# Optimization experiments

Measured on AMD Instinct MI355X. Metric: run time of the kernel, lower is better.

Reference implementation:

```python
import jax, jax.numpy as jnp
import numpy as np

K = 16
EPS = 1e-5

def _conv1x1(w, b, x):
    # w: [O, I], x: [B, I, N] -> [B, O, N]
    return jnp.einsum('oi,bin->bon', w, x) + b[None, :, None]

def _bn(g, be, m, v, x):
    # inference-mode batchnorm over channel dim of [B, C, N]
    inv = g / jnp.sqrt(v + EPS)
    return x * inv[None, :, None] + (be - m * inv)[None, :, None]

def setup_inputs() -> dict:
    key = jax.random.key(0)
    ks = jax.random.split(key, 16)
    B, C, N = 2, 128, 8192
    d = {}
    d['x'] = jax.random.normal(ks[0], (B, C, N), jnp.float32)
    d['xyz'] = jax.random.normal(ks[1], (B, N, 3), jnp.float32)
    def conv(k, o, i):
        k1, k2 = jax.random.split(k)
        s = 1.0 / np.sqrt(i)
        return (jax.random.uniform(k1, (o, i), jnp.float32, -s, s),
                jax.random.uniform(k2, (o,), jnp.float32, -s, s))
    def bn(k, c):
        return (jax.random.uniform(k, (c,), jnp.float32, 0.5, 1.5),
                jnp.zeros((c,), jnp.float32), jnp.zeros((c,), jnp.float32), jnp.ones((c,), jnp.float32))
    # boundary_net: 2C->C (bn,relu), C->C (bn,relu)
    d['bw1'], d['bb1'] = conv(ks[2], C, 2 * C)
    d['bn1g'], d['bn1b'], d['bn1m'], d['bn1v'] = bn(ks[3], C)
    d['bw2'], d['bb2'] = conv(ks[4], C, C)
    d['bn2g'], d['bn2b'], d['bn2m'], d['bn2v'] = bn(ks[5], C)
    # spatial_relation: 4->32 (bn,relu), 32->64
    d['sw1'], d['sb1'] = conv(ks[6], 32, 4)
    d['sbng'], d['sbnb'], d['sbnm'], d['sbnv'] = bn(ks[7], 32)
    d['sw2'], d['sb2'] = conv(ks[8], 64, 32)
    # attention: C+64 -> C//2 (bn,relu), C//2 -> C, sigmoid
    d['aw1'], d['ab1'] = conv(ks[9], C // 2, C + 64)
    d['abng'], d['abnb'], d['abnm'], d['abnv'] = bn(ks[10], C // 2)
    d['aw2'], d['ab2'] = conv(ks[11], C, C // 2)
    return d

def reference(x, xyz, bw1, bb1, bn1g, bn1b, bn1m, bn1v, bw2, bb2, bn2g, bn2b, bn2m, bn2v,
              sw1, sb1, sbng, sbnb, sbnm, sbnv, sw2, sb2,
              aw1, ab1, abng, abnb, abnm, abnv, aw2, ab2):
    B, C, N = x.shape
    # pairwise squared distances [B, N, N]
    xx = jnp.sum(xyz * xyz, axis=2)  # [B, N]
    dist = xx[:, :, None] + xx[:, None, :] - 2.0 * jnp.einsum('bnd,bmd->bnm', xyz, xyz)
    _, knn_idx = jax.lax.top_k(-dist, K)  # [B, N, K], K smallest distances
    # gather neighbor coords [B, N, K, 3]
    knn_xyz = jax.vmap(lambda p, i: p[i])(xyz, knn_idx)
    rel = knn_xyz - xyz[:, :, None, :]                  # [B, N, K, 3]
    rel_d = jnp.sqrt(jnp.sum(rel * rel, axis=-1))       # [B, N, K]
    mean_rel = jnp.mean(rel, axis=2).transpose(0, 2, 1)   # [B, 3, N]
    mean_d = jnp.mean(rel_d, axis=2)[:, None, :]           # [B, 1, N]
    spatial = jnp.concatenate([mean_rel, mean_d], axis=1)  # [B, 4, N]
    s = jax.nn.relu(_bn(sbng, sbnb, sbnm, sbnv, _conv1x1(sw1, sb1, spatial)))
    spatial_feat = _conv1x1(sw2, sb2, s)  # [B, 64, N]
    # gather neighbor features [B, C, N, K]
    knn_feat = jax.vmap(lambda xb, ib: xb[:, ib])(x, knn_idx)
    max_diff = jnp.max(knn_feat - x[:, :, :, None], axis=3)  # [B, C, N]
    bf = jnp.concatenate([x, max_diff], axis=1)  # [B, 2C, N]
    bf = jax.nn.relu(_bn(bn1g, bn1b, bn1m, bn1v, _conv1x1(bw1, bb1, bf)))
    boundary_feat = jax.nn.relu(_bn(bn2g, bn2b, bn2m, bn2v, _conv1x1(bw2, bb2, bf)))
    ai = jnp.concatenate([x, spatial_feat], axis=1)  # [B, C+64, N]
    a = jax.nn.relu(_bn(abng, abnb, abnm, abnv, _conv1x1(aw1, ab1, ai)))
    attn = jax.nn.sigmoid(_conv1x1(aw2, ab2, a))  # [B, C, N]
    return x + boundary_feat * attn
```

## Files before the change

kernel.cpp:

```cpp
#include <hip/hip_runtime.h>
#include <math.h>

#define NPTS  8192
#define NB    2
#define NTOT  (NPTS*NB)
#define GD    60
#define NCELL (GD*GD*GD)
#define TOTC  (NB*NCELL)
#define HCELL 0.2f
#define INVH  5.0f
#define ORGN  (-6.0f)
#define NN    8192
#define SCAN_CHUNK 1024
#define NBLK_SCAN  ((TOTC + SCAN_CHUNK - 1) / SCAN_CHUNK)
#define RSTART    2
#define RESC      4
#define SEL_CAP  1024

#define OFF_CNT     ((size_t)0)
#define OFF_OFFS    (OFF_CNT    + (size_t)TOTC*4)
#define OFF_CELLID  (OFF_OFFS   + (size_t)TOTC*4)
#define OFF_RANK    (OFF_CELLID + (size_t)NTOT*4)
#define OFF_SPOS    (OFF_RANK   + (size_t)NTOT*4)
#define OFF_KNN     (OFF_SPOS   + (size_t)NTOT*16)
#define OFF_SPATIAL (OFF_KNN    + (size_t)NTOT*16*4)
#define OFF_XT      (OFF_SPATIAL+ (size_t)NB*4*NPTS*4)
#define OFF_MD      (OFF_XT     + (size_t)NB*128*NPTS*4)
#define OFF_S1      (OFF_MD     + (size_t)NB*128*NPTS*4)
#define OFF_SF      (OFF_S1     + (size_t)NB*32*NPTS*4)
#define OFF_Y1      (OFF_SF     + (size_t)NB*64*NPTS*4)
#define OFF_Y2      (OFF_Y1     + (size_t)NB*128*NPTS*4)
#define OFF_A1      (OFF_Y2     + (size_t)NB*128*NPTS*4)
#define OFF_SC      (OFF_A1     + (size_t)NB*64*NPTS*4)
#define OFF_BSUM    (OFF_SC     + (size_t)1088*4)
#define OFF_BPRE    (OFF_BSUM   + (size_t)NBLK_SCAN*4)
#define OFF_RNG     (((OFF_BPRE + (size_t)NBLK_SCAN*4) + 15) & ~(size_t)15)

static __device__ __forceinline__ float sumsq3(float x, float y, float z) {
    return __fadd_rn(__fadd_rn(__fmul_rn(x, x), __fmul_rn(y, y)), __fmul_rn(z, z));
}
static __device__ __forceinline__ float pdist4(float qx, float qy, float qz, float qxx,
                                               float px, float py, float pz) {
    float pxx = sumsq3(px, py, pz);
    float dot = __fadd_rn(__fadd_rn(__fmul_rn(qx, px), __fmul_rn(qy, py)), __fmul_rn(qz, pz));
    return __fsub_rn(__fadd_rn(qxx, pxx), __fadd_rn(dot, dot));
}
static __device__ __forceinline__ unsigned fkey(float f) {
    unsigned b = __float_as_uint(f);
    return b ^ ((unsigned)(((int)b) >> 31) | 0x80000000u);
}
static __device__ __forceinline__ unsigned long long shflx64(unsigned long long v, int m) {
    unsigned lo = __shfl_xor((unsigned)v, m, 64);
    unsigned hi = __shfl_xor((unsigned)(v >> 32), m, 64);
    return ((unsigned long long)hi << 32) | lo;
}
static __device__ __forceinline__ int wave_scan_incl(int v, int lane) {
    #pragma unroll
    for (int d = 1; d < 64; d <<= 1) {
        int u = __shfl_up(v, d, 64);
        v += (lane >= d) ? u : 0;
    }
    return v;
}
static __device__ __forceinline__ unsigned long long tkmake(float m) {
    return ((unsigned long long)(fkey(__fsub_rn(__fmul_rn(m, m), 1e-4f)) + 1u)) << 27;
}

__global__ void cell_build(const float* __restrict__ xyz, int* __restrict__ cnt,
                           int* __restrict__ cellid, int* __restrict__ rank) {
    int t = blockIdx.x * 256 + threadIdx.x;
    if (t >= NTOT) return;
    const float* p = xyz + (size_t)t * 3;
    float x = p[0], y = p[1], z = p[2];
    int cx = min(GD - 1, max(0, (int)floorf((x - ORGN) * INVH)));
    int cy = min(GD - 1, max(0, (int)floorf((y - ORGN) * INVH)));
    int cz = min(GD - 1, max(0, (int)floorf((z - ORGN) * INVH)));
    int gcell = (t >> 13) * NCELL + (cz * GD + cy) * GD + cx;
    rank[t] = atomicAdd(&cnt[gcell], 1);
    cellid[t] = gcell;
}

__global__ __launch_bounds__(256) void scan_sums(const int* __restrict__ cnt, int* __restrict__ bsum) {
    __shared__ int red[256];
    int blk = blockIdx.x, t = threadIdx.x;
    int i0 = blk * SCAN_CHUNK + t * 4;
    int s = 0;
    if (i0 + 3 < TOTC) {
        int4 v = *(const int4*)(cnt + i0);
        s = v.x + v.y + v.z + v.w;
    } else {
        for (int j = 0; j < 4; ++j) if (i0 + j < TOTC) s += cnt[i0 + j];
    }
    red[t] = s;
    __syncthreads();
    for (int d = 128; d > 0; d >>= 1) {
        if (t < d) red[t] += red[t + d];
        __syncthreads();
    }
    if (t == 0) bsum[blk] = red[0];
}

__global__ __launch_bounds__(512) void scan_top(const int* __restrict__ bsum, int* __restrict__ bpre) {
    __shared__ int ps[512];
    int t = threadIdx.x;
    int v = (t < NBLK_SCAN) ? bsum[t] : 0;
    ps[t] = v;
    __syncthreads();
    for (int d = 1; d < 512; d <<= 1) {
        int u = 0;
        if (t >= d) u = ps[t - d];
        __syncthreads();
        ps[t] += u;
        __syncthreads();
    }
    if (t < NBLK_SCAN) bpre[t] = ps[t] - v;
}

__global__ __launch_bounds__(256) void scan_write(const int* __restrict__ cnt, const int* __restrict__ bpre,
                                                  int* __restrict__ offs, int2* __restrict__ rng) {
    __shared__ int ps[256];
    int blk = blockIdx.x, t = threadIdx.x;
    int i0 = blk * SCAN_CHUNK + t * 4;
    int a = 0, b = 0, c = 0, d = 0;
    if (i0 + 3 < TOTC) {
        int4 v = *(const int4*)(cnt + i0);
        a = v.x; b = v.y; c = v.z; d = v.w;
    } else {
        if (i0 + 0 < TOTC) a = cnt[i0 + 0];
        if (i0 + 1 < TOTC) b = cnt[i0 + 1];
        if (i0 + 2 < TOTC) c = cnt[i0 + 2];
        if (i0 + 3 < TOTC) d = cnt[i0 + 3];
    }
    int s = a + b + c + d;
    ps[t] = s;
    __syncthreads();
    for (int dd = 1; dd < 256; dd <<= 1) {
        int u = 0;
        if (t >= dd) u = ps[t - dd];
        __syncthreads();
        ps[t] += u;
        __syncthreads();
    }
    int base = bpre[blk] + ps[t] - s;
    if (i0 + 3 < TOTC) {
        offs[i0 + 0] = base;
        offs[i0 + 1] = base + a;
        offs[i0 + 2] = base + a + b;
        offs[i0 + 3] = base + a + b + c;
        *(int4*)(rng + i0)     = make_int4(base, base + a, base + a, base + a + b);
        *(int4*)(rng + i0 + 2) = make_int4(base + a + b, base + a + b + c,
                                           base + a + b + c, base + s);
    } else {
        if (i0 + 0 < TOTC) { offs[i0 + 0] = base;             rng[i0 + 0] = make_int2(base, base + a); }
        if (i0 + 1 < TOTC) { offs[i0 + 1] = base + a;         rng[i0 + 1] = make_int2(base + a, base + a + b); }
        if (i0 + 2 < TOTC) { offs[i0 + 2] = base + a + b;     rng[i0 + 2] = make_int2(base + a + b, base + a + b + c); }
        if (i0 + 3 < TOTC) { offs[i0 + 3] = base + a + b + c; rng[i0 + 3] = make_int2(base + a + b + c, base + s); }
    }
}

__global__ void scatter_k(const float* __restrict__ xyz, const int* __restrict__ cellid,
                          const int* __restrict__ rank, const int* __restrict__ offs,
                          float4* __restrict__ spos) {
    int t = blockIdx.x * 256 + threadIdx.x;
    if (t >= NTOT) return;
    const float* p = xyz + (size_t)t * 3;
    float x = p[0], y = p[1], z = p[2];
    int pos = offs[cellid[t]] + rank[t];
    spos[pos] = make_float4(x, y, z, __int_as_float(t & (NPTS - 1)));
}

__global__ __launch_bounds__(64) void knn_kernel(const float4* __restrict__ spos,
                                                 const int2* __restrict__ rng,
                                                 int* __restrict__ knn,
                                                 float* __restrict__ spatial) {
    __shared__ __align__(16) unsigned long long sel[SEL_CAP];
    __shared__ __align__(16) unsigned long long sel2[512];
    int lane = threadIdx.x;
    int bid  = blockIdx.x;
    int s = (bid & 7) * (NTOT / 8) + (bid >> 3);
    float4 q = spos[s];
    float qx = q.x, qy = q.y, qz = q.z;
    float qxx = sumsq3(qx, qy, qz);
    int b  = s >> 13;
    int nq = __float_as_int(q.w);
    int cx = min(GD - 1, max(0, (int)floorf((qx - ORGN) * INVH)));
    int cy = min(GD - 1, max(0, (int)floorf((qy - ORGN) * INVH)));
    int cz = min(GD - 1, max(0, (int)floorf((qz - ORGN) * INVH)));
    const int2* rg = rng + b * NCELL;

    float mlx = qx - (ORGN + (float)cx * HCELL);
    float mhx = (ORGN + (float)(cx + 1) * HCELL) - qx;
    float mly = qy - (ORGN + (float)cy * HCELL);
    float mhy = (ORGN + (float)(cy + 1) * HCELL) - qy;
    float mlz = qz - (ORGN + (float)cz * HCELL);
    float mhz = (ORGN + (float)(cz + 1) * HCELL) - qz;
    float margin0 = fminf(fminf(fminf(mlx, mhx), fminf(mly, mhy)), fminf(mlz, mhz));

    int tot = 0, ovf = 0;

    auto scan_ball = [&](int RB, float mfin, unsigned long long tkfin) {
        if (mfin <= 0.f) return;
        float mfin2 = mfin * mfin;
        int L = 2 * RB + 1, nrows = L * L;
        for (int r0 = 0; r0 < nrows; r0 += 64) {
            int nr = min(64, nrows - r0);
            int rr = r0 + lane;
            int num = 0, start = 0;
            if (rr < nrows) {
                int dzr = rr / L - RB, dyr = rr % L - RB;
                int zc = cz + dzr, yc = cy + dyr;
                if ((unsigned)zc < GD && (unsigned)yc < GD) {
                    float ylo = ORGN + (float)yc * HCELL;
                    float zlo = ORGN + (float)zc * HCELL;
                    float dyl = fmaxf(fmaxf(ylo - qy, qy - (ylo + HCELL)), 0.f);
                    float dzl = fmaxf(fmaxf(zlo - qz, qz - (zlo + HCELL)), 0.f);
                    float rem = mfin2 - dyl * dyl - dzl * dzl;
                    if (rem > -1e-4f) {
                        float xh = sqrtf(fmaxf(rem, 0.f)) + 1e-3f;
                        int xlo = max(0, (int)floorf((qx - xh - ORGN) * INVH));
                        int xhi = min(GD - 1, (int)floorf((qx + xh - ORGN) * INVH));
                        if (xlo <= xhi) {
                            int rowb = (zc * GD + yc) * GD;
                            start = rg[rowb + xlo].x;
                            num   = rg[rowb + xhi].y - start;
                        }
                    }
                }
            }
            int inc = wave_scan_incl(num, lane);
            int ctot = __shfl(inc, 63, 64);
            if (ctot == 0) continue;
            int excl = inc - num;
            auto eg = [&](int base, int& sv, float4& pv, bool& vld) {
                int t = base + lane;
                vld = t < ctot;
                int tc = vld ? t : (ctot - 1);
                int lo = 0, hi = nr - 1;
                #pragma unroll
                for (int st = 0; st < 6; ++st) {
                    int mid = (lo + hi + 1) >> 1;
                    int e = __shfl(excl, mid, 64);
                    bool g = (e <= tc);
                    lo = g ? mid : lo;
                    hi = g ? hi : (mid - 1);
                }
                sv = __shfl(start, lo, 64) + (tc - __shfl(excl, lo, 64));
                pv = spos[sv];
            };
            int s0; float4 p0; bool v0;
            eg(0, s0, p0, v0);
            for (int base = 0; base < ctot; base += 64) {
                int s1 = 0; float4 p1 = p0; bool v1 = false;
                if (base + 64 < ctot) eg(base + 64, s1, p1, v1);
                float d = pdist4(qx, qy, qz, qxx, p0.x, p0.y, p0.z);
                unsigned long long key = ((unsigned long long)fkey(d) << 27)
                                       | ((unsigned long long)(unsigned)__float_as_int(p0.w) << 14)
                                       | (unsigned)s0;
                bool pass = v0 && (key < tkfin);
                unsigned long long mk = __ballot(pass);
                int cnum = (int)__popcll(mk);
                if (tot + cnum > SEL_CAP) { ovf = 1; return; }
                if (pass) sel[tot + (int)__popcll(mk & ((1ULL << lane) - 1ULL))] = key;
                tot += cnum;
                s0 = s1; p0 = p1; v0 = v1;
            }
        }
    };

    auto count_below = [&](unsigned long long tk) {
        int c = 0;
        for (int t0 = 0; t0 < tot; t0 += 64) {
            int tt = t0 + lane;
            if (tt < tot) c += (sel[tt] < tk) ? 1 : 0;
        }
        for (int o = 32; o > 0; o >>= 1) c += __shfl_xor(c, o, 64);
        return c;
    };

    float mfin1 = margin0 + (float)RSTART * HCELL;
    unsigned long long tkf1 = (mfin1 > 0.f) ? tkmake(mfin1) : 0ULL;
    if (tkf1) scan_ball(RSTART, mfin1, tkf1);

    unsigned long long tkey_sel = ~0ULL;
    int csel = 0;
    bool have = false;
    if (!ovf && tot >= 16) {
        float mA = margin0 + 1.0f * HCELL;
        if (mA > 0.f) {
            unsigned long long tkA = tkmake(mA);
            int cA = count_below(tkA);
            if (cA >= 16) { tkey_sel = tkA; csel = cA; have = true; }
        }
        if (!have) { tkey_sel = ~0ULL; csel = tot; have = true; }
    }
    if (!have && !ovf) {
        tot = 0;
        float mfin4 = margin0 + (float)RESC * HCELL;
        unsigned long long tkf4 = (mfin4 > 0.f) ? tkmake(mfin4) : 0ULL;
        if (tkf4) scan_ball(RESC, mfin4, tkf4);
        if (!ovf && tot >= 16) {
            float mB = margin0 + (float)(RESC - 1) * HCELL;
            if (mB > 0.f) {
                unsigned long long tkB = tkmake(mB);
                int cB = count_below(tkB);
                if (cB >= 16) { tkey_sel = tkB; csel = cB; have = true; }
            }
            if (!have) { tkey_sel = ~0ULL; csel = tot; have = true; }
        }
    }

    if (!have) {
        const float LADR[16] = {0.35f, 0.4725f, 0.637875f, 0.86113125f,
                                1.1625272f, 1.5694117f, 2.1187058f, 2.8602529f,
                                3.8613414f, 5.2128109f, 7.0372947f, 9.5003478f,
                                12.825470f, 17.314384f, 23.374418f, 31.555464f};
        int sbase = b << 13;
        int cc[16];
        #pragma unroll
        for (int k = 0; k < 16; ++k) cc[k] = 0;
        for (int i0 = 0; i0 < NPTS; i0 += 64) {
            float4 p = spos[sbase + i0 + lane];
            float d = pdist4(qx, qy, qz, qxx, p.x, p.y, p.z);
            #pragma unroll
            for (int k = 0; k < 16; ++k) cc[k] += (d < LADR[k] * LADR[k]) ? 1 : 0;
        }
        #pragma unroll
        for (int k = 0; k < 16; ++k)
            for (int o = 32; o > 0; o >>= 1) cc[k] += __shfl_xor(cc[k], o, 64);
        float Tq = LADR[15] * LADR[15]; int cL = cc[15];
        #pragma unroll
        for (int k = 14; k >= 0; --k) if (cc[k] >= 16) { Tq = LADR[k] * LADR[k]; cL = cc[k]; }
        if (cL <= SEL_CAP) {
            tot = 0;
            for (int i0 = 0; i0 < NPTS; i0 += 64) {
                int idx = sbase + i0 + lane;
                float4 p = spos[idx];
                float d = pdist4(qx, qy, qz, qxx, p.x, p.y, p.z);
                bool pass = (d < Tq);
                unsigned long long key = ((unsigned long long)fkey(d) << 27)
                                       | ((unsigned long long)(unsigned)__float_as_int(p.w) << 14)
                                       | (unsigned)idx;
                unsigned long long mk = __ballot(pass);
                if (pass) sel[tot + (int)__popcll(mk & ((1ULL << lane) - 1ULL))] = key;
                tot += (int)__popcll(mk);
            }
            tkey_sel = ~0ULL;
            csel = tot;
        } else {
            unsigned long long* mybuf = sel + lane;
            unsigned long long minkey = ~0ULL, maxkey = 0;
            int nbuf = 0;
            for (int i = lane; i < NPTS; i += 64) {
                float4 p = spos[sbase + i];
                float d = pdist4(qx, qy, qz, qxx, p.x, p.y, p.z);
                unsigned long long key = ((unsigned long long)fkey(d) << 27)
                                       | ((unsigned long long)(unsigned)__float_as_int(p.w) << 14)
                                       | (unsigned)(sbase + i);
                if (nbuf < 16) {
                    mybuf[(size_t)nbuf * 64] = key;
                    ++nbuf;
                    minkey = (key < minkey) ? key : minkey;
                    maxkey = (key > maxkey) ? key : maxkey;
                } else if (key < maxkey) {
                    unsigned long long vmax = 0, v2 = 0;
                    int pmax = 0;
                    #pragma unroll
                    for (int j = 0; j < 16; ++j) {
                        unsigned long long v = mybuf[(size_t)j * 64];
                        if (v > vmax) { v2 = vmax; vmax = v; pmax = j; }
                        else if (v > v2) { v2 = v; }
                    }
                    mybuf[(size_t)pmax * 64] = key;
                    maxkey = (key > v2) ? key : v2;
                    minkey = (key < minkey) ? key : minkey;
                }
            }
            unsigned long long keep = ~0ULL;
            for (int k = 0; k < 16; ++k) {
                unsigned long long m = minkey;
                for (int o = 32; o > 0; o >>= 1) {
                    unsigned long long pv = shflx64(m, o);
                    m = (pv < m) ? pv : m;
                }
                unsigned long long bal = __ballot(minkey == m);
                int wl = __ffsll((long long)bal) - 1;
                if (lane == wl) {
                    int pos = 0;
                    for (int j = 0; j < nbuf; ++j) if (mybuf[(size_t)j * 64] == m) pos = j;
                    --nbuf;
                    mybuf[(size_t)pos * 64] = mybuf[(size_t)nbuf * 64];
                    unsigned long long nm = ~0ULL;
                    for (int j = 0; j < nbuf; ++j) {
                        unsigned long long v = mybuf[(size_t)j * 64];
                        nm = (v < nm) ? v : nm;
                    }
                    minkey = nm;
                }
                if (lane == k) keep = m;
            }
            float rx = 0.f, ry = 0.f, rz = 0.f, rd = 0.f;
            if (lane < 16) {
                int sp = (int)(keep & 0x3FFFu);
                int oi = (int)((keep >> 14) & 0x1FFFu);
                float4 p = spos[sp];
                rx = p.x - qx; ry = p.y - qy; rz = p.z - qz;
                rd = sqrtf(__fadd_rn(__fadd_rn(__fmul_rn(rx, rx), __fmul_rn(ry, ry)), __fmul_rn(rz, rz)));
                knn[(((size_t)b << 13) + nq) * 16 + lane] = oi;
            }
            for (int o = 8; o > 0; o >>= 1) {
                rx += __shfl_xor(rx, o, 64);
                ry += __shfl_xor(ry, o, 64);
                rz += __shfl_xor(rz, o, 64);
                rd += __shfl_xor(rd, o, 64);
            }
            if (lane == 0) {
                const float inv16 = 0.0625f;
                spatial[((size_t)b * 4 + 0) * NPTS + nq] = rx * inv16;
                spatial[((size_t)b * 4 + 1) * NPTS + nq] = ry * inv16;
                spatial[((size_t)b * 4 + 2) * NPTS + nq] = rz * inv16;
                spatial[((size_t)b * 4 + 3) * NPTS + nq] = rd * inv16;
            }
            return;
        }
    }

    const unsigned long long* src = sel;
    int m = tot;
    if (tkey_sel != ~0ULL && csel <= 512) {
        int w = 0;
        for (int t0 = 0; t0 < tot; t0 += 64) {
            int tt = t0 + lane;
            unsigned long long v = (tt < tot) ? sel[tt] : ~0ULL;
            bool pass = (tt < tot) && (v < tkey_sel);
            unsigned long long mk = __ballot(pass);
            if (pass) sel2[w + (int)__popcll(mk & ((1ULL << lane) - 1ULL))] = v;
            w += (int)__popcll(mk);
        }
        asm volatile("s_waitcnt lgkmcnt(0)" ::: "memory");
        __builtin_amdgcn_sched_barrier(0);
        src = sel2; m = w;
        tkey_sel = ~0ULL;
    }
    float rxs = 0.f, rys = 0.f, rzs = 0.f, rds = 0.f;
    for (int t0 = 0; t0 < m; t0 += 64) {
        int tt = t0 + lane;
        if (tt < m) {
            unsigned long long kt = src[tt];
            if (kt < tkey_sel) {
                int rr = 0;
                for (int j = 0; j < m; ++j) rr += (src[j] < kt) ? 1 : 0;
                if (rr < 16) {
                    int sp = (int)(kt & 0x3FFFu);
                    int oi = (int)((kt >> 14) & 0x1FFFu);
                    float4 p = spos[sp];
                    float dx = p.x - qx, dy = p.y - qy, dz = p.z - qz;
                    float dl = sqrtf(__fadd_rn(__fadd_rn(__fmul_rn(dx, dx), __fmul_rn(dy, dy)), __fmul_rn(dz, dz)));
                    knn[(((size_t)b << 13) + nq) * 16 + rr] = oi;
                    rxs += dx; rys += dy; rzs += dz; rds += dl;
                }
            }
        }
    }
    for (int o = 32; o > 0; o >>= 1) {
        rxs += __shfl_xor(rxs, o, 64);
        rys += __shfl_xor(rys, o, 64);
        rzs += __shfl_xor(rzs, o, 64);
        rds += __shfl_xor(rds, o, 64);
    }
    if (lane == 0) {
        const float inv16 = 0.0625f;
        spatial[((size_t)b * 4 + 0) * NPTS + nq] = rxs * inv16;
        spatial[((size_t)b * 4 + 1) * NPTS + nq] = rys * inv16;
        spatial[((size_t)b * 4 + 2) * NPTS + nq] = rzs * inv16;
        spatial[((size_t)b * 4 + 3) * NPTS + nq] = rds * inv16;
    }
}

__global__ void transpose_k(const float* __restrict__ x, float* __restrict__ xT) {
    __shared__ float tl[32][33];
    int b = blockIdx.z;
    int n0 = blockIdx.x * 32, c0 = blockIdx.y * 32;
    int tx = threadIdx.x, ty = threadIdx.y;
    const float* xb = x + (size_t)b * 128 * NN;
    float* xtb = xT + (size_t)b * NN * 128;
    for (int i = 0; i < 32; i += 8) tl[ty + i][tx] = xb[(size_t)(c0 + ty + i) * NN + n0 + tx];
    __syncthreads();
    for (int i = 0; i < 32; i += 8) xtb[(size_t)(n0 + ty + i) * 128 + c0 + tx] = tl[tx][ty + i];
}

__global__ __launch_bounds__(256) void md_k(const float* __restrict__ xT,
                                            const int* __restrict__ knn,
                                            float* __restrict__ md) {
    __shared__ int ki[8][16];
    __shared__ float smd[8][132];
    int b = blockIdx.y;
    int n0 = blockIdx.x * 8;
    int tid = threadIdx.x;
    if (tid < 128) ki[tid >> 4][tid & 15] = knn[(((size_t)b << 13) + n0 + (tid >> 4)) * 16 + (tid & 15)];
    __syncthreads();
    int nl = tid >> 5;
    int c4 = (tid & 31) * 4;
    const float* xb = xT + (size_t)b * NPTS * 128;
    float4 m = make_float4(-3.0e38f, -3.0e38f, -3.0e38f, -3.0e38f);
    #pragma unroll
    for (int k = 0; k < 16; ++k) {
        const float4 g = *(const float4*)(xb + (size_t)ki[nl][k] * 128 + c4);
        m.x = fmaxf(m.x, g.x); m.y = fmaxf(m.y, g.y); m.z = fmaxf(m.z, g.z); m.w = fmaxf(m.w, g.w);
    }
    const float4 own = *(const float4*)(xb + (size_t)(n0 + nl) * 128 + c4);
    m.x -= own.x; m.y -= own.y; m.z -= own.z; m.w -= own.w;
    *(float4*)(&smd[nl][c4]) = m;
    __syncthreads();
    for (int r = 0; r < 4; ++r) {
        int c = (tid >> 3) + 32 * r;
        int n2 = tid & 7;
        md[((size_t)b * 128 + c) * NN + n0 + n2] = smd[n2][c];
    }
}

__global__ void prep_k(const float* bb1, const float* g1, const float* be1, const float* m1, const float* v1,
                       const float* bb2, const float* g2, const float* be2, const float* m2, const float* v2,
                       const float* sb1, const float* gs,  const float* bes, const float* ms, const float* vs,
                       const float* sb2,
                       const float* ab1, const float* ga,  const float* bea, const float* ma, const float* va,
                       const float* ab2, float* sc) {
    int t = threadIdx.x;
    if (t < 128) {
        float i1 = g1[t] / sqrtf(v1[t] + 1e-5f);
        sc[t] = i1;        sc[128 + t] = bb1[t] * i1 + be1[t] - m1[t] * i1;
        float i2 = g2[t] / sqrtf(v2[t] + 1e-5f);
        sc[256 + t] = i2;  sc[384 + t] = bb2[t] * i2 + be2[t] - m2[t] * i2;
        sc[832 + t] = 1.0f; sc[960 + t] = ab2[t];
    }
    if (t < 32) {
        float is = gs[t] / sqrtf(vs[t] + 1e-5f);
        sc[512 + t] = is;  sc[544 + t] = sb1[t] * is + bes[t] - ms[t] * is;
    }
    if (t < 64) {
        sc[576 + t] = 1.0f; sc[640 + t] = sb2[t];
        float ia = ga[t] / sqrtf(va[t] + 1e-5f);
        sc[704 + t] = ia;  sc[768 + t] = ab1[t] * ia + bea[t] - ma[t] * ia;
    }
}

template <int O, int K, int TILE_N, int SPLIT, int ACT>
__global__ __launch_bounds__(256) void conv_bn(const float* __restrict__ srcA,
                                               const float* __restrict__ srcB,
                                               const float* __restrict__ W,
                                               const float* __restrict__ scale,
                                               const float* __restrict__ shift,
                                               float* __restrict__ out,
                                               const float* __restrict__ resx,
                                               const float* __restrict__ y2,
                                               float* __restrict__ dout) {
    constexpr int KC  = (K < 64) ? K : 64;
    constexpr int NT4 = TILE_N / 4;
    constexpr int O4  = O / 4;
    static_assert(NT4 * O4 == 256, "thread mapping");
    __shared__ float wT[KC][O + 4];
    __shared__ float inT[KC][TILE_N];
    int tid = threadIdx.x;
    int b = blockIdx.z;
    int n0 = blockIdx.x * TILE_N;
    int n_thr = tid % NT4;
    int o_thr = tid / NT4;
    float acc[4][4] = {{0.f, 0.f, 0.f, 0.f}, {0.f, 0.f, 0.f, 0.f}, {0.f, 0.f, 0.f, 0.f}, {0.f, 0.f, 0.f, 0.f}};

    for (int k0 = 0; k0 < K; k0 += KC) {
        for (int idx = tid; idx < KC * O; idx += 256) {
            int cc = idx % KC;
            int o  = idx / KC;
            wT[cc][o] = W[(size_t)o * K + k0 + cc];
        }
        for (int idx = tid; idx < KC * NT4; idx += 256) {
            int cc = idx / NT4;
            int nf = idx % NT4;
            int cg = k0 + cc;
            const float* src = (cg < SPLIT)
                ? (srcA + ((size_t)b * SPLIT + cg) * NN)
                : (srcB + ((size_t)b * (K - SPLIT) + (cg - SPLIT)) * NN);
            *(float4*)(&inT[cc][nf * 4]) = *(const float4*)(src + n0 + nf * 4);
        }
        __syncthreads();
        #pragma unroll 8
        for (int c = 0; c < KC; ++c) {
            float4 wv = *(const float4*)(&wT[c][o_thr * 4]);
            float4 iv = *(const float4*)(&inT[c][n_thr * 4]);
            acc[0][0] = fmaf(wv.x, iv.x, acc[0][0]); acc[0][1] = fmaf(wv.x, iv.y, acc[0][1]);
            acc[0][2] = fmaf(wv.x, iv.z, acc[0][2]); acc[0][3] = fmaf(wv.x, iv.w, acc[0][3]);
            acc[1][0] = fmaf(wv.y, iv.x, acc[1][0]); acc[1][1] = fmaf(wv.y, iv.y, acc[1][1]);
            acc[1][2] = fmaf(wv.y, iv.z, acc[1][2]); acc[1][3] = fmaf(wv.y, iv.w, acc[1][3]);
            acc[2][0] = fmaf(wv.z, iv.x, acc[2][0]); acc[2][1] = fmaf(wv.z, iv.y, acc[2][1]);
            acc[2][2] = fmaf(wv.z, iv.z, acc[2][2]); acc[2][3] = fmaf(wv.z, iv.w, acc[2][3]);
            acc[3][0] = fmaf(wv.w, iv.x, acc[3][0]); acc[3][1] = fmaf(wv.w, iv.y, acc[3][1]);
            acc[3][2] = fmaf(wv.w, iv.z, acc[3][2]); acc[3][3] = fmaf(wv.w, iv.w, acc[3][3]);
        }
        __syncthreads();
    }
    #pragma unroll
    for (int j = 0; j < 4; ++j) {
        int o = o_thr * 4 + j;
        float scv = scale[o], shv = shift[o];
        float4 v;
        v.x = fmaf(acc[j][0], scv, shv);
        v.y = fmaf(acc[j][1], scv, shv);
        v.z = fmaf(acc[j][2], scv, shv);
        v.w = fmaf(acc[j][3], scv, shv);
        size_t obase = ((size_t)b * O + o) * NN + n0 + n_thr * 4;
        if (ACT == 1) {
            v.x = fmaxf(v.x, 0.f); v.y = fmaxf(v.y, 0.f); v.z = fmaxf(v.z, 0.f); v.w = fmaxf(v.w, 0.f);
            *(float4*)(out + obase) = v;
        } else if (ACT == 2) {
            float4 xr = *(const float4*)(resx + obase);
            float4 yr = *(const float4*)(y2 + obase);
            v.x = xr.x + yr.x / (1.f + __expf(-v.x));
            v.y = xr.y + yr.y / (1.f + __expf(-v.y));
            v.z = xr.z + yr.z / (1.f + __expf(-v.z));
            v.w = xr.w + yr.w / (1.f + __expf(-v.w));
            *(float4*)(dout + obase) = v;
        } else {
            *(float4*)(out + obase) = v;
        }
    }
}

extern "C" void kernel_launch(void* const* d_in, const int* in_sizes, int n_in,
                              void* d_out, int out_size, void* d_ws, size_t ws_size,
                              hipStream_t stream) {
    (void)in_sizes; (void)n_in; (void)out_size; (void)ws_size;
    const float* x    = (const float*)d_in[0];
    const float* xyz  = (const float*)d_in[1];
    const float* bw1  = (const float*)d_in[2];
    const float* bb1  = (const float*)d_in[3];
    const float* bn1g = (const float*)d_in[4];
    const float* bn1b = (const float*)d_in[5];
    const float* bn1m = (const float*)d_in[6];
    const float* bn1v = (const float*)d_in[7];
    const float* bw2  = (const float*)d_in[8];
    const float* bb2  = (const float*)d_in[9];
    const float* bn2g = (const float*)d_in[10];
    const float* bn2b = (const float*)d_in[11];
    const float* bn2m = (const float*)d_in[12];
    const float* bn2v = (const float*)d_in[13];
    const float* sw1  = (const float*)d_in[14];
    const float* sb1  = (const float*)d_in[15];
    const float* sbng = (const float*)d_in[16];
    const float* sbnb = (const float*)d_in[17];
    const float* sbnm = (const float*)d_in[18];
    const float* sbnv = (const float*)d_in[19];
    const float* sw2  = (const float*)d_in[20];
    const float* sb2  = (const float*)d_in[21];
    const float* aw1  = (const float*)d_in[22];
    const float* ab1  = (const float*)d_in[23];
    const float* abng = (const float*)d_in[24];
    const float* abnb = (const float*)d_in[25];
    const float* abnm = (const float*)d_in[26];
    const float* abnv = (const float*)d_in[27];
    const float* aw2  = (const float*)d_in[28];
    const float* ab2  = (const float*)d_in[29];

    char* ws = (char*)d_ws;
    int*    cnt    = (int*)(ws + OFF_CNT);
    int*    offs   = (int*)(ws + OFF_OFFS);
    int*    cellid = (int*)(ws + OFF_CELLID);
    int*    rank   = (int*)(ws + OFF_RANK);
    float4* spos   = (float4*)(ws + OFF_SPOS);
    int*    knn    = (int*)(ws + OFF_KNN);
    float*  spat   = (float*)(ws + OFF_SPATIAL);
    float*  xT     = (float*)(ws + OFF_XT);
    float*  md     = (float*)(ws + OFF_MD);
    float*  s1b    = (float*)(ws + OFF_S1);
    float*  sfb    = (float*)(ws + OFF_SF);
    float*  y1b    = (float*)(ws + OFF_Y1);
    float*  y2b    = (float*)(ws + OFF_Y2);
    float*  a1b    = (float*)(ws + OFF_A1);
    float*  sc     = (float*)(ws + OFF_SC);
    int*    bsum   = (int*)(ws + OFF_BSUM);
    int*    bpre   = (int*)(ws + OFF_BPRE);
    int2*   rng    = (int2*)(ws + OFF_RNG);
    float*  dout   = (float*)d_out;

    hipMemsetAsync(cnt, 0, (size_t)TOTC * 4, stream);
    cell_build<<<dim3((NTOT + 255) / 256), 256, 0, stream>>>(xyz, cnt, cellid, rank);
    scan_sums<<<dim3(NBLK_SCAN), 256, 0, stream>>>(cnt, bsum);
    scan_top<<<dim3(1), 512, 0, stream>>>(bsum, bpre);
    scan_write<<<dim3(NBLK_SCAN), 256, 0, stream>>>(cnt, bpre, offs, rng);
    scatter_k<<<dim3((NTOT + 255) / 256), 256, 0, stream>>>(xyz, cellid, rank, offs, spos);
    knn_kernel<<<dim3(NTOT), 64, 0, stream>>>(spos, rng, knn, spat);
    transpose_k<<<dim3(NPTS / 32, 128 / 32, NB), dim3(32, 8), 0, stream>>>(x, xT);
    md_k<<<dim3(NPTS / 8, NB), 256, 0, stream>>>(xT, knn, md);
    prep_k<<<1, 128, 0, stream>>>(bb1, bn1g, bn1b, bn1m, bn1v,
                                  bb2, bn2g, bn2b, bn2m, bn2v,
                                  sb1, sbng, sbnb, sbnm, sbnv,
                                  sb2,
                                  ab1, abng, abnb, abnm, abnv,
                                  ab2, sc);
    conv_bn<32, 4, 128, 4, 1><<<dim3(NPTS / 128, 1, NB), 256, 0, stream>>>(
        spat, spat, sw1, sc + 512, sc + 544, s1b, nullptr, nullptr, nullptr);
    conv_bn<64, 32, 64, 32, 0><<<dim3(NPTS / 64, 1, NB), 256, 0, stream>>>(
        s1b, s1b, sw2, sc + 576, sc + 640, sfb, nullptr, nullptr, nullptr);
    conv_bn<128, 256, 32, 128, 1><<<dim3(NPTS / 32, 1, NB), 256, 0, stream>>>(
        x, md, bw1, sc + 0, sc + 128, y1b, nullptr, nullptr, nullptr);
    conv_bn<128, 128, 32, 128, 1><<<dim3(NPTS / 32, 1, NB), 256, 0, stream>>>(
        y1b, y1b, bw2, sc + 256, sc + 384, y2b, nullptr, nullptr, nullptr);
    conv_bn<64, 192, 64, 128, 1><<<dim3(NPTS / 64, 1, NB), 256, 0, stream>>>(
        x, sfb, aw1, sc + 704, sc + 768, a1b, nullptr, nullptr, nullptr);
    conv_bn<128, 64, 32, 64, 2><<<dim3(NPTS / 32, 1, NB), 256, 0, stream>>>(
        a1b, a1b, aw2, sc + 832, sc + 960, dout, x, y2b, dout);
}
```

Before: 326.0 us.

## Fuse back-to-back 1x1 conv pairs keeping intermediates in shared memory

Replaces the four separate conv_bn launches for the boundary and attention MLPs with two fused kernels. Each fused kernel computes the first conv+BN+ReLU into a shared-memory tile, then applies the second conv directly from that tile. This removes the global round-trip of the y1 and a1 intermediates and two kernel launches. The cost is larger shared-memory footprints (about 66KB for boundary), which may lower occupancy, plus reloading weights for every point tile.

```diff
diff --git a/kernel.cpp b/kernel.cpp
--- a/kernel.cpp
+++ b/kernel.cpp
@@ -549,10 +549,7 @@
                                                const float* __restrict__ W,
                                                const float* __restrict__ scale,
                                                const float* __restrict__ shift,
-                                               float* __restrict__ out,
-                                               const float* __restrict__ resx,
-                                               const float* __restrict__ y2,
-                                               float* __restrict__ dout) {
+                                               float* __restrict__ out) {
     constexpr int KC  = (K < 64) ? K : 64;
     constexpr int NT4 = TILE_N / 4;
     constexpr int O4  = O / 4;
@@ -609,18 +606,190 @@
         size_t obase = ((size_t)b * O + o) * NN + n0 + n_thr * 4;
         if (ACT == 1) {
             v.x = fmaxf(v.x, 0.f); v.y = fmaxf(v.y, 0.f); v.z = fmaxf(v.z, 0.f); v.w = fmaxf(v.w, 0.f);
-            *(float4*)(out + obase) = v;
-        } else if (ACT == 2) {
-            float4 xr = *(const float4*)(resx + obase);
-            float4 yr = *(const float4*)(y2 + obase);
+        }
+        *(float4*)(out + obase) = v;
+    }
+}
+
+#define FMA16(ACCV, WV, IV) \
+    ACCV[0][0] = fmaf(WV.x, IV.x, ACCV[0][0]); ACCV[0][1] = fmaf(WV.x, IV.y, ACCV[0][1]); \
+    ACCV[0][2] = fmaf(WV.x, IV.z, ACCV[0][2]); ACCV[0][3] = fmaf(WV.x, IV.w, ACCV[0][3]); \
+    ACCV[1][0] = fmaf(WV.y, IV.x, ACCV[1][0]); ACCV[1][1] = fmaf(WV.y, IV.y, ACCV[1][1]); \
+    ACCV[1][2] = fmaf(WV.y, IV.z, ACCV[1][2]); ACCV[1][3] = fmaf(WV.y, IV.w, ACCV[1][3]); \
+    ACCV[2][0] = fmaf(WV.z, IV.x, ACCV[2][0]); ACCV[2][1] = fmaf(WV.z, IV.y, ACCV[2][1]); \
+    ACCV[2][2] = fmaf(WV.z, IV.z, ACCV[2][2]); ACCV[2][3] = fmaf(WV.z, IV.w, ACCV[2][3]); \
+    ACCV[3][0] = fmaf(WV.w, IV.x, ACCV[3][0]); ACCV[3][1] = fmaf(WV.w, IV.y, ACCV[3][1]); \
+    ACCV[3][2] = fmaf(WV.w, IV.z, ACCV[3][2]); ACCV[3][3] = fmaf(WV.w, IV.w, ACCV[3][3])
+
+__global__ __launch_bounds__(256) void fused_boundary(const float* __restrict__ x,
+                                                      const float* __restrict__ md,
+                                                      const float* __restrict__ W1,
+                                                      const float* __restrict__ W2,
+                                                      const float* __restrict__ sc,
+                                                      float* __restrict__ y2b) {
+    __shared__ float wT[64][132];
+    __shared__ float inT[64][32];
+    __shared__ float y1t[128][32];
+    int tid = threadIdx.x;
+    int b = blockIdx.z;
+    int n0 = blockIdx.x * 32;
+    int n_thr = tid % 8;
+    int o_thr = tid / 8;
+    float acc[4][4] = {{0.f,0.f,0.f,0.f},{0.f,0.f,0.f,0.f},{0.f,0.f,0.f,0.f},{0.f,0.f,0.f,0.f}};
+
+    for (int k0 = 0; k0 < 256; k0 += 64) {
+        for (int idx = tid; idx < 64 * 128; idx += 256) {
+            int cc = idx % 64;
+            int o  = idx / 64;
+            wT[cc][o] = W1[(size_t)o * 256 + k0 + cc];
+        }
+        for (int idx = tid; idx < 64 * 8; idx += 256) {
+            int cc = idx / 8;
+            int nf = idx % 8;
+            int cg = k0 + cc;
+            const float* src = (cg < 128)
+                ? (x  + ((size_t)b * 128 + cg) * NN)
+                : (md + ((size_t)b * 128 + (cg - 128)) * NN);
+            *(float4*)(&inT[cc][nf * 4]) = *(const float4*)(src + n0 + nf * 4);
+        }
+        __syncthreads();
+        #pragma unroll 8
+        for (int c = 0; c < 64; ++c) {
+            float4 wv = *(const float4*)(&wT[c][o_thr * 4]);
+            float4 iv = *(const float4*)(&inT[c][n_thr * 4]);
+            FMA16(acc, wv, iv);
+        }
+        __syncthreads();
+    }
+    #pragma unroll
+    for (int j = 0; j < 4; ++j) {
+        int o = o_thr * 4 + j;
+        float scv = sc[o], shv = sc[128 + o];
+        float4 v;
+        v.x = fmaxf(fmaf(acc[j][0], scv, shv), 0.f);
+        v.y = fmaxf(fmaf(acc[j][1], scv, shv), 0.f);
+        v.z = fmaxf(fmaf(acc[j][2], scv, shv), 0.f);
+        v.w = fmaxf(fmaf(acc[j][3], scv, shv), 0.f);
+        *(float4*)(&y1t[o][n_thr * 4]) = v;
+    }
+    __syncthreads();
+
+    float a2[4][4] = {{0.f,0.f,0.f,0.f},{0.f,0.f,0.f,0.f},{0.f,0.f,0.f,0.f},{0.f,0.f,0.f,0.f}};
+    for (int k0 = 0; k0 < 128; k0 += 64) {
+        for (int idx = tid; idx < 64 * 128; idx += 256) {
+            int cc = idx % 64;
+            int o  = idx / 64;
+            wT[cc][o] = W2[(size_t)o * 128 + k0 + cc];
+        }
+        __syncthreads();
+        #pragma unroll 8
+        for (int c = 0; c < 64; ++c) {
+            float4 wv = *(const float4*)(&wT[c][o_thr * 4]);
+            float4 iv = *(const float4*)(&y1t[k0 + c][n_thr * 4]);
+            FMA16(a2, wv, iv);
+        }
+        __syncthreads();
+    }
+    #pragma unroll
+    for (int j = 0; j < 4; ++j) {
+        int o = o_thr * 4 + j;
+        float scv = sc[256 + o], shv = sc[384 + o];
+        float4 v;
+        v.x = fmaxf(fmaf(a2[j][0], scv, shv), 0.f);
+        v.y = fmaxf(fmaf(a2[j][1], scv, shv), 0.f);
+        v.z = fmaxf(fmaf(a2[j][2], scv, shv), 0.f);
+        v.w = fmaxf(fmaf(a2[j][3], scv, shv), 0.f);
+        *(float4*)(y2b + ((size_t)b * 128 + o) * NN + n0 + n_thr * 4) = v;
+    }
+}
+
+__global__ __launch_bounds__(256) void fused_attn(const float* __restrict__ x,
+                                                  const float* __restrict__ sfb,
+                                                  const float* __restrict__ W1,
+                                                  const float* __restrict__ W2,
+                                                  const float* __restrict__ sc,
+                                                  const float* __restrict__ y2b,
+                                                  float* __restrict__ dout) {
+    __shared__ float wT[64][68];
+    __shared__ float inT[64][64];
+    __shared__ float a1t[64][64];
+    int tid = threadIdx.x;
+    int b = blockIdx.z;
+    int n0 = blockIdx.x * 64;
+    int n_thr = tid % 16;
+    int o_thr = tid / 16;
+    float acc[4][4] = {{0.f,0.f,0.f,0.f},{0.f,0.f,0.f,0.f},{0.f,0.f,0.f,0.f},{0.f,0.f,0.f,0.f}};
+
+    for (int k0 = 0; k0 < 192; k0 += 64) {
+        for (int idx = tid; idx < 64 * 64; idx += 256) {
+            int cc = idx % 64;
+            int o  = idx / 64;
+            wT[cc][o] = W1[(size_t)o * 192 + k0 + cc];
+        }
+        for (int idx = tid; idx < 64 * 16; idx += 256) {
+            int cc = idx / 16;
+            int nf = idx % 16;
+            int cg = k0 + cc;
+            const float* src = (cg < 128)
+                ? (x   + ((size_t)b * 128 + cg) * NN)
+                : (sfb + ((size_t)b * 64 + (cg - 128)) * NN);
+            *(float4*)(&inT[cc][nf * 4]) = *(const float4*)(src + n0 + nf * 4);
+        }
+        __syncthreads();
+        #pragma unroll 8
+        for (int c = 0; c < 64; ++c) {
+            float4 wv = *(const float4*)(&wT[c][o_thr * 4]);
+            float4 iv = *(const float4*)(&inT[c][n_thr * 4]);
+            FMA16(acc, wv, iv);
+        }
+        __syncthreads();
+    }
+    #pragma unroll
+    for (int j = 0; j < 4; ++j) {
+        int o = o_thr * 4 + j;
+        float scv = sc[704 + o], shv = sc[768 + o];
+        float4 v;
+        v.x = fmaxf(fmaf(acc[j][0], scv, shv), 0.f);
+        v.y = fmaxf(fmaf(acc[j][1], scv, shv), 0.f);
+        v.z = fmaxf(fmaf(acc[j][2], scv, shv), 0.f);
+        v.w = fmaxf(fmaf(acc[j][3], scv, shv), 0.f);
+        *(float4*)(&a1t[o][n_thr * 4]) = v;
+    }
+    __syncthreads();
+
+    for (int oh = 0; oh < 128; oh += 64) {
+        for (int idx = tid; idx < 64 * 64; idx += 256) {
+            int cc = idx % 64;
+            int o  = idx / 64;
+            wT[cc][o] = W2[(size_t)(oh + o) * 64 + cc];
+        }
+        __syncthreads();
+        float a2[4][4] = {{0.f,0.f,0.f,0.f},{0.f,0.f,0.f,0.f},{0.f,0.f,0.f,0.f},{0.f,0.f,0.f,0.f}};
+        #pragma unroll 8
+        for (int c = 0; c < 64; ++c) {
+            float4 wv = *(const float4*)(&wT[c][o_thr * 4]);
+            float4 iv = *(const float4*)(&a1t[c][n_thr * 4]);
+            FMA16(a2, wv, iv);
+        }
+        #pragma unroll
+        for (int j = 0; j < 4; ++j) {
+            int o = oh + o_thr * 4 + j;
+            float scv = sc[832 + o], shv = sc[960 + o];
+            float4 v;
+            v.x = fmaf(a2[j][0], scv, shv);
+            v.y = fmaf(a2[j][1], scv, shv);
+            v.z = fmaf(a2[j][2], scv, shv);
+            v.w = fmaf(a2[j][3], scv, shv);
+            size_t obase = ((size_t)b * 128 + o) * NN + n0 + n_thr * 4;
+            float4 xr = *(const float4*)(x + obase);
+            float4 yr = *(const float4*)(y2b + obase);
             v.x = xr.x + yr.x / (1.f + __expf(-v.x));
             v.y = xr.y + yr.y / (1.f + __expf(-v.y));
             v.z = xr.z + yr.z / (1.f + __expf(-v.z));
             v.w = xr.w + yr.w / (1.f + __expf(-v.w));
             *(float4*)(dout + obase) = v;
-        } else {
-            *(float4*)(out + obase) = v;
-        }
+        }
+        __syncthreads();
     }
 }
 
@@ -671,9 +840,7 @@
     float*  md     = (float*)(ws + OFF_MD);
     float*  s1b    = (float*)(ws + OFF_S1);
     float*  sfb    = (float*)(ws + OFF_SF);
-    float*  y1b    = (float*)(ws + OFF_Y1);
     float*  y2b    = (float*)(ws + OFF_Y2);
-    float*  a1b    = (float*)(ws + OFF_A1);
     float*  sc     = (float*)(ws + OFF_SC);
     int*    bsum   = (int*)(ws + OFF_BSUM);
     int*    bpre   = (int*)(ws + OFF_BPRE);
@@ -696,15 +863,9 @@
                                   ab1, abng, abnb, abnm, abnv,
                                   ab2, sc);
     conv_bn<32, 4, 128, 4, 1><<<dim3(NPTS / 128, 1, NB), 256, 0, stream>>>(
-        spat, spat, sw1, sc + 512, sc + 544, s1b, nullptr, nullptr, nullptr);
+        spat, spat, sw1, sc + 512, sc + 544, s1b);
     conv_bn<64, 32, 64, 32, 0><<<dim3(NPTS / 64, 1, NB), 256, 0, stream>>>(
-        s1b, s1b, sw2, sc + 576, sc + 640, sfb, nullptr, nullptr, nullptr);
-    conv_bn<128, 256, 32, 128, 1><<<dim3(NPTS / 32, 1, NB), 256, 0, stream>>>(
-        x, md, bw1, sc + 0, sc + 128, y1b, nullptr, nullptr, nullptr);
-    conv_bn<128, 128, 32, 128, 1><<<dim3(NPTS / 32, 1, NB), 256, 0, stream>>>(
-        y1b, y1b, bw2, sc + 256, sc + 384, y2b, nullptr, nullptr, nullptr);
-    conv_bn<64, 192, 64, 128, 1><<<dim3(NPTS / 64, 1, NB), 256, 0, stream>>>(
-        x, sfb, aw1, sc + 704, sc + 768, a1b, nullptr, nullptr, nullptr);
-    conv_bn<128, 64, 32, 64, 2><<<dim3(NPTS / 32, 1, NB), 256, 0, stream>>>(
-        a1b, a1b, aw2, sc + 832, sc + 960, dout, x, y2b, dout);
-}
+        s1b, s1b, sw2, sc + 576, sc + 640, sfb);
+    fused_boundary<<<dim3(NPTS / 32, 1, NB), 256, 0, stream>>>(x, md, bw1, bw2, sc, y2b);
+    fused_attn<<<dim3(NPTS / 64, 1, NB), 256, 0, stream>>>(x, sfb, aw1, aw2, sc, y2b, dout);
+}
```

Result: no change. 321.6 us (-1.4%).
